# Kernel tuning notes

Hardware: AMD Instinct MI355X
Metric: run time of the kernel (lower is better)

The kernel has to match this reference:

```python
import jax, jax.numpy as jnp
import numpy as np

N = 20000      # nodes
E = 640000     # edges (before self-loops)
F = 64         # base node feature len
H = 2          # heads per layer
EPS = 1e-5
NEG_SLOPE = 0.2  # PyG GATConv leaky_relu slope


def setup_inputs():
    key = jax.random.key(0)
    ks = jax.random.split(key, 16)
    s = 0.1
    x = jax.random.normal(ks[0], (N, F), jnp.float32)
    edge_index = jax.random.randint(ks[1], (2, E), 0, N, dtype=jnp.int64)
    # layer 1: in=F, heads=H, out-per-head C1=F -> out dim H*F=128
    C1 = F
    W1 = jax.random.normal(ks[2], (F, H * C1), jnp.float32) * s
    att_src1 = jax.random.normal(ks[3], (H, C1), jnp.float32) * s
    att_dst1 = jax.random.normal(ks[4], (H, C1), jnp.float32) * s
    bias1 = jnp.zeros((H * C1,), jnp.float32)
    gamma1 = jnp.ones((H * C1,), jnp.float32)
    beta1 = jnp.zeros((H * C1,), jnp.float32)
    # layer 2: in=H*F=128, heads=H, out-per-head C2=H*F -> out dim H*H*F=256
    C2 = H * F
    W2 = jax.random.normal(ks[5], (H * C1, H * C2), jnp.float32) * s
    att_src2 = jax.random.normal(ks[6], (H, C2), jnp.float32) * s
    att_dst2 = jax.random.normal(ks[7], (H, C2), jnp.float32) * s
    bias2 = jnp.zeros((H * C2,), jnp.float32)
    gamma2 = jnp.ones((H * C2,), jnp.float32)
    beta2 = jnp.zeros((H * C2,), jnp.float32)
    return {"x": x, "edge_index": edge_index,
            "W1": W1, "att_src1": att_src1, "att_dst1": att_dst1, "bias1": bias1,
            "gamma1": gamma1, "beta1": beta1,
            "W2": W2, "att_src2": att_src2, "att_dst2": att_dst2, "bias2": bias2,
            "gamma2": gamma2, "beta2": beta2}


def _gat_conv(x, src, dst, W, att_src, att_dst, bias):
    # PyG GATConv (concat=True, add_self_loops already applied to src/dst)
    n = x.shape[0]
    h, c = att_src.shape
    hx = (x @ W).reshape(n, h, c)                       # [N,H,C]
    a_s = jnp.einsum('nhc,hc->nh', hx, att_src)         # [N,H]
    a_d = jnp.einsum('nhc,hc->nh', hx, att_dst)
    e = a_s[src] + a_d[dst]                             # [E',H]
    e = jnp.where(e > 0, e, NEG_SLOPE * e)              # leaky relu
    # segment softmax over incoming edges of each target node
    m = jax.ops.segment_max(e, dst, num_segments=n)     # [N,H]
    p = jnp.exp(e - m[dst])
    z = jax.ops.segment_sum(p, dst, num_segments=n)     # [N,H]
    alpha = p / z[dst]                                  # [E',H]
    msg = hx[src] * alpha[:, :, None]                   # [E',H,C]
    out = jax.ops.segment_sum(msg, dst, num_segments=n) # [N,H,C]
    return out.reshape(n, h * c) + bias


def _batch_norm(x, gamma, beta):
    mu = x.mean(axis=0)
    var = x.var(axis=0)  # biased, matches torch BN normalization
    return (x - mu) * jax.lax.rsqrt(var + EPS) * gamma + beta


def reference(x, edge_index, W1, att_src1, att_dst1, bias1, gamma1, beta1,
              W2, att_src2, att_dst2, bias2, gamma2, beta2):
    loops = jnp.arange(N, dtype=edge_index.dtype)
    src = jnp.concatenate([edge_index[0], loops])
    dst = jnp.concatenate([edge_index[1], loops])
    h = _gat_conv(x, src, dst, W1, att_src1, att_dst1, bias1)
    h = jax.nn.relu(_batch_norm(h, gamma1, beta1))
    h = _gat_conv(h, src, dst, W2, att_src2, att_dst2, bias2)
    h = jax.nn.relu(_batch_norm(h, gamma2, beta2))
    return h
```

## Files before the change

kernel.cpp:

```cpp
#include <hip/hip_runtime.h>
#include <hip/hip_bf16.h>
#include <math.h>

#define NN 20000
#define ER 640000
#define ET 660000
#define HH 2
#define D1 128
#define D2 256
#define EPSV 1e-5f
#define SLOPE 0.2f

typedef __attribute__((ext_vector_type(8))) short bf16x8;
typedef __attribute__((ext_vector_type(4))) float f32x4;


__device__ __forceinline__ int detect64(const void* ei) {
  const int* p = (const int*)ei;
  return (p[1] | p[3] | p[5] | p[7]) == 0;
}
__device__ __forceinline__ int clampn(int v) { return v < 0 ? 0 : (v >= NN ? NN-1 : v); }
__device__ __forceinline__ float bf16_lo(unsigned int u){ return __uint_as_float(u<<16); }
__device__ __forceinline__ float bf16_hi(unsigned int u){ return __uint_as_float(u & 0xffff0000u); }

__global__ void k_front(const void* ei, const float* W1, const float* W2,
                        __hip_bfloat16* W1t, __hip_bfloat16* W2c, int* dpart, int* gcount) {
  extern __shared__ int hist[];
  int b = blockIdx.x, t = threadIdx.x;
  if (b == 0 && t == 0) *gcount = 0;
  if (b < 160) {
    int i = b*256 + t;
    if (i < 8192) {
      int n = i >> 6, k = i & 63;
      W1t[i] = __float2bfloat16(W1[k*128 + n]);
    } else {
      int i2 = i - 8192;
      int kc = i2 >> 13, n = (i2 >> 5) & 255, kk = i2 & 31;
      W2c[i2] = __float2bfloat16(W2[(kc*32 + kk)*256 + n]);
    }
    return;
  }
  int db = b - 160;
  for (int i = t; i < NN; i += 256) hist[i] = 0;
  __syncthreads();
  int is64 = detect64(ei);
  int base = db * 80000;
  if (is64) {
    const long long* p64 = (const long long*)ei;
    for (int i = base + t*4; i < base + 80000; i += 1024) {
      uint4 qa = *(const uint4*)(p64 + ER + i);
      uint4 qb = *(const uint4*)(p64 + ER + i + 2);
      atomicAdd(&hist[clampn((int)qa.x)], 1);
      atomicAdd(&hist[clampn((int)qa.z)], 1);
      atomicAdd(&hist[clampn((int)qb.x)], 1);
      atomicAdd(&hist[clampn((int)qb.z)], 1);
    }
  } else {
    const int* p32 = (const int*)ei;
    for (int i = base + t*4; i < base + 80000; i += 1024) {
      uint4 q = *(const uint4*)(p32 + ER + i);
      atomicAdd(&hist[clampn((int)q.x)], 1);
      atomicAdd(&hist[clampn((int)q.y)], 1);
      atomicAdd(&hist[clampn((int)q.z)], 1);
      atomicAdd(&hist[clampn((int)q.w)], 1);
    }
  }
  __syncthreads();
  for (int i = t; i < NN; i += 256) dpart[db*NN + i] = hist[i];
}

__global__ __launch_bounds__(256) void k_alloc(const int* dpart, int* begv, int* endv,
                                               int* cursor, int* gcount, float* bnz) {
  __shared__ int wsum[4], wbase[4];
  int gid = blockIdx.x*256 + threadIdx.x;
  if (gid < 768) bnz[gid] = 0.f;
  int d = 0;
  if (gid < NN) {
    d = 1;
    #pragma unroll
    for (int bb = 0; bb < 8; bb++) d += dpart[bb*NN + gid];
  }
  int lane = threadIdx.x & 63, w = threadIdx.x >> 6;
  int v = d;
  #pragma unroll
  for (int o = 1; o < 64; o <<= 1) {
    int u = __shfl_up(v, o);
    if (lane >= o) v += u;
  }
  if (lane == 63) wsum[w] = v;
  __syncthreads();
  if (threadIdx.x == 0) {
    int s0 = wsum[0], s1 = wsum[1], s2 = wsum[2], s3 = wsum[3];
    int b = atomicAdd(gcount, s0 + s1 + s2 + s3);
    wbase[0] = b; wbase[1] = b + s0; wbase[2] = b + s0 + s1; wbase[3] = b + s0 + s1 + s2;
  }
  __syncthreads();
  if (gid < NN) {
    int beg = wbase[w] + v - d;
    begv[gid] = beg; cursor[gid] = beg; endv[gid] = beg + d;
  }
}

__global__ void k_scatter(const void* ei, int* cursor, int* srcs) {
  int i0 = (blockIdx.x*256 + threadIdx.x)*4;
  if (i0 >= ET) return;
  int s[4], d[4];
  if (i0 >= ER) {
    #pragma unroll
    for (int k = 0; k < 4; k++) { s[k] = i0 + k - ER; d[k] = s[k]; }
  } else if (detect64(ei)) {
    const long long* p64 = (const long long*)ei;
    uint4 qa = *(const uint4*)(p64 + i0);
    uint4 qb = *(const uint4*)(p64 + i0 + 2);
    uint4 ra = *(const uint4*)(p64 + ER + i0);
    uint4 rb = *(const uint4*)(p64 + ER + i0 + 2);
    s[0]=clampn((int)qa.x); s[1]=clampn((int)qa.z); s[2]=clampn((int)qb.x); s[3]=clampn((int)qb.z);
    d[0]=clampn((int)ra.x); d[1]=clampn((int)ra.z); d[2]=clampn((int)rb.x); d[3]=clampn((int)rb.z);
  } else {
    const int* p32 = (const int*)ei;
    uint4 qs = *(const uint4*)(p32 + i0);
    uint4 qd = *(const uint4*)(p32 + ER + i0);
    s[0]=clampn((int)qs.x); s[1]=clampn((int)qs.y); s[2]=clampn((int)qs.z); s[3]=clampn((int)qs.w);
    d[0]=clampn((int)qd.x); d[1]=clampn((int)qd.y); d[2]=clampn((int)qd.z); d[3]=clampn((int)qd.w);
  }
  #pragma unroll
  for (int k = 0; k < 4; k++) {
    int pos = atomicAdd(&cursor[d[k]], 1);
    srcs[pos] = s[k];
  }
}

__global__ __launch_bounds__(256) void k_gemm1f(const float* x, const __hip_bfloat16* W1t,
                                                const float* att_s1, const float* att_d1,
                                                __hip_bfloat16* hxb, float2* as1, float2* ad1) {
  __shared__ __hip_bfloat16 As[64][72];
  __shared__ __hip_bfloat16 Bs[128][72];
  __shared__ float asred[4][64], adred[4][64];
  int t = threadIdx.x;
  int m0 = blockIdx.x * 64;
  for (int i = t; i < 512; i += 256) {
    int r = i >> 3, s = i & 7;
    int gr = m0 + r; if (gr >= NN) gr = NN - 1;
    float4 f0 = ((const float4*)(x + (size_t)gr*64))[s*2];
    float4 f1 = ((const float4*)(x + (size_t)gr*64))[s*2+1];
    __hip_bfloat16 hb[8] = {
      __float2bfloat16(f0.x), __float2bfloat16(f0.y), __float2bfloat16(f0.z), __float2bfloat16(f0.w),
      __float2bfloat16(f1.x), __float2bfloat16(f1.y), __float2bfloat16(f1.z), __float2bfloat16(f1.w)};
    *(uint4*)&As[r][s*8] = *(uint4*)hb;
  }
  for (int i = t; i < 1024; i += 256) {
    int r = i >> 3, s = i & 7;
    *(uint4*)&Bs[r][s*8] = ((const uint4*)(W1t + (size_t)r*64))[s];
  }
  __syncthreads();
  int w = t >> 6, lane = t & 63;
  int lm = lane & 15, q = lane >> 4;
  f32x4 acc[4][2];
  #pragma unroll
  for (int rt = 0; rt < 4; rt++)
    #pragma unroll
    for (int ct = 0; ct < 2; ct++) acc[rt][ct] = (f32x4){0.f,0.f,0.f,0.f};
  #pragma unroll
  for (int kc = 0; kc < 2; kc++) {
    bf16x8 bfr[2];
    #pragma unroll
    for (int ct = 0; ct < 2; ct++)
      bfr[ct] = *(const bf16x8*)&Bs[w*32 + ct*16 + lm][kc*32 + q*8];
    #pragma unroll
    for (int rt = 0; rt < 4; rt++) {
      bf16x8 a = *(const bf16x8*)&As[rt*16 + lm][kc*32 + q*8];
      acc[rt][0] = __builtin_amdgcn_mfma_f32_16x16x32_bf16(a, bfr[0], acc[rt][0], 0, 0, 0);
      acc[rt][1] = __builtin_amdgcn_mfma_f32_16x16x32_bf16(a, bfr[1], acc[rt][1], 0, 0, 0);
    }
  }
  #pragma unroll
  for (int rt = 0; rt < 4; rt++)
    #pragma unroll
    for (int ct = 0; ct < 2; ct++)
      #pragma unroll
      for (int rg = 0; rg < 4; rg++) {
        int row = m0 + rt*16 + q*4 + rg;
        int col = w*32 + ct*16 + lm;
        if (row < NN) hxb[(size_t)row*128 + col] = __float2bfloat16(acc[rt][ct][rg]);
      }
  float asc[2], adc[2];
  #pragma unroll
  for (int ct = 0; ct < 2; ct++) {
    int col = w*32 + ct*16 + lm;
    asc[ct] = att_s1[col]; adc[ct] = att_d1[col];
  }
  #pragma unroll
  for (int rt = 0; rt < 4; rt++)
    #pragma unroll
    for (int rg = 0; rg < 4; rg++) {
      float ps = acc[rt][0][rg]*asc[0] + acc[rt][1][rg]*asc[1];
      float pd = acc[rt][0][rg]*adc[0] + acc[rt][1][rg]*adc[1];
      #pragma unroll
      for (int o = 1; o < 16; o <<= 1) { ps += __shfl_xor(ps, o); pd += __shfl_xor(pd, o); }
      if (lm == 0) { int row = rt*16 + q*4 + rg; asred[w][row] = ps; adred[w][row] = pd; }
    }
  __syncthreads();
  if (t < 64) {
    int row = m0 + t;
    if (row < NN) {
      as1[row] = make_float2(asred[0][t] + asred[1][t], asred[2][t] + asred[3][t]);
      ad1[row] = make_float2(adred[0][t] + adred[1][t], adred[2][t] + adred[3][t]);
    }
  }
}

__global__ __launch_bounds__(256) void k_gemm2f(const float* out1, const __hip_bfloat16* W2c,
                                                const float* bns1, const float* bnq1,
                                                const float* gamma1, const float* beta1,
                                                const float* att_s2, const float* att_d2,
                                                __hip_bfloat16* hxb, float2* as2, float2* ad2) {
  __shared__ __hip_bfloat16 As[64][136];
  __shared__ __hip_bfloat16 Bs[256][40];
  __shared__ float AB[2][128];
  __shared__ float asred[4][64], adred[4][64];
  int t = threadIdx.x;
  int m0 = blockIdx.x * 64;
  if (t < 128) {
    float mean = bns1[t]*(1.f/NN);
    float var  = bnq1[t]*(1.f/NN) - mean*mean;
    float A = rsqrtf(var + EPSV)*gamma1[t];
    AB[0][t] = A; AB[1][t] = beta1[t] - mean*A;
  }
  __syncthreads();
  for (int i = t; i < 1024; i += 256) {
    int r = i >> 4, s = i & 15;
    int gr = m0 + r; if (gr >= NN) gr = NN - 1;
    float4 f0 = ((const float4*)(out1 + (size_t)gr*128))[s*2];
    float4 f1 = ((const float4*)(out1 + (size_t)gr*128))[s*2+1];
    int c = s*8;
    float v[8] = {f0.x,f0.y,f0.z,f0.w,f1.x,f1.y,f1.z,f1.w};
    __hip_bfloat16 hb[8];
    #pragma unroll
    for (int k = 0; k < 8; k++)
      hb[k] = __float2bfloat16(fmaxf(v[k]*AB[0][c+k] + AB[1][c+k], 0.f));
    *(uint4*)&As[r][s*8] = *(uint4*)hb;
  }
  int w = t >> 6, lane = t & 63;
  int lm = lane & 15, q = lane >> 4;
  f32x4 acc[4][4];
  #pragma unroll
  for (int rt = 0; rt < 4; rt++)
    #pragma unroll
    for (int ct = 0; ct < 4; ct++) acc[rt][ct] = (f32x4){0.f,0.f,0.f,0.f};
  for (int kc = 0; kc < 4; kc++) {
    __syncthreads();
    for (int i = t; i < 1024; i += 256) {
      int r = i >> 2, s = i & 3;
      *(uint4*)&Bs[r][s*8] = ((const uint4*)(W2c + ((size_t)kc*256 + r)*32))[s];
    }
    __syncthreads();
    bf16x8 bfr[4];
    #pragma unroll
    for (int ct = 0; ct < 4; ct++)
      bfr[ct] = *(const bf16x8*)&Bs[w*64 + ct*16 + lm][q*8];
    #pragma unroll
    for (int rt = 0; rt < 4; rt++) {
      bf16x8 a = *(const bf16x8*)&As[rt*16 + lm][kc*32 + q*8];
      #pragma unroll
      for (int ct = 0; ct < 4; ct++)
        acc[rt][ct] = __builtin_amdgcn_mfma_f32_16x16x32_bf16(a, bfr[ct], acc[rt][ct], 0, 0, 0);
    }
  }
  #pragma unroll
  for (int rt = 0; rt < 4; rt++)
    #pragma unroll
    for (int ct = 0; ct < 4; ct++)
      #pragma unroll
      for (int rg = 0; rg < 4; rg++) {
        int row = m0 + rt*16 + q*4 + rg;
        int col = w*64 + ct*16 + lm;
        if (row < NN) hxb[(size_t)row*256 + col] = __float2bfloat16(acc[rt][ct][rg]);
      }
  float asc[4], adc[4];
  #pragma unroll
  for (int ct = 0; ct < 4; ct++) {
    int col = w*64 + ct*16 + lm;
    asc[ct] = att_s2[col]; adc[ct] = att_d2[col];
  }
  #pragma unroll
  for (int rt = 0; rt < 4; rt++)
    #pragma unroll
    for (int rg = 0; rg < 4; rg++) {
      float ps = acc[rt][0][rg]*asc[0] + acc[rt][1][rg]*asc[1]
               + acc[rt][2][rg]*asc[2] + acc[rt][3][rg]*asc[3];
      float pd = acc[rt][0][rg]*adc[0] + acc[rt][1][rg]*adc[1]
               + acc[rt][2][rg]*adc[2] + acc[rt][3][rg]*adc[3];
      #pragma unroll
      for (int o = 1; o < 16; o <<= 1) { ps += __shfl_xor(ps, o); pd += __shfl_xor(pd, o); }
      if (lm == 0) { int row = rt*16 + q*4 + rg; asred[w][row] = ps; adred[w][row] = pd; }
    }
  __syncthreads();
  if (t < 64) {
    int row = m0 + t;
    if (row < NN) {
      as2[row] = make_float2(asred[0][t] + asred[1][t], asred[2][t] + asred[3][t]);
      ad2[row] = make_float2(adred[0][t] + adred[1][t], adred[2][t] + adred[3][t]);
    }
  }
}

__global__ __launch_bounds__(64) void k_agg1(const int* begv, const int* endv, const int* srcs,
                                             const float2* asv, const float2* adv,
                                             const uint2* hx, const float* bias, float* out) {
  __shared__ float2 sp[2][64];
  int n = blockIdx.x, t = threadIdx.x;
  int l = t & 31, eo = t >> 5;
  int h = l >> 4;
  float2 ad = adv[n];
  int beg = begv[n], end = endv[n];
  float a0=0.f,a1=0.f,a2=0.f,a3=0.f,z0=0.f,z1=0.f;
  for (int cb = beg; cb < end; cb += 64) {
    int len = end - cb; if (len > 64) len = 64;
    if (t < len) {
      int s = srcs[cb + t];
      float2 as = asv[s];
      float e0 = as.x + ad.x, e1 = as.y + ad.y;
      e0 = e0 > 0.f ? e0 : SLOPE*e0;
      e1 = e1 > 0.f ? e1 : SLOPE*e1;
      float p0 = __expf(e0), p1 = __expf(e1);
      sp[0][t] = make_float2(__int_as_float(s), p0);
      sp[1][t] = make_float2(__int_as_float(s), p1);
      z0 += p0; z1 += p1;
    }
    __syncthreads();
    for (int j = eo; j < len; j += 2) {
      float2 v = sp[h][j];
      uint2 u = hx[(size_t)__float_as_int(v.x)*32 + l];
      a0 += v.y*bf16_lo(u.x); a1 += v.y*bf16_hi(u.x);
      a2 += v.y*bf16_lo(u.y); a3 += v.y*bf16_hi(u.y);
    }
    __syncthreads();
  }
  a0 += __shfl_down(a0, 32); a1 += __shfl_down(a1, 32);
  a2 += __shfl_down(a2, 32); a3 += __shfl_down(a3, 32);
  #pragma unroll
  for (int o = 1; o < 64; o <<= 1) { z0 += __shfl_xor(z0, o); z1 += __shfl_xor(z1, o); }
  if (t < 32) {
    float inv = 1.f / (h ? z1 : z0);
    float4 b4 = ((const float4*)bias)[t];
    float4 o4 = { a0*inv + b4.x, a1*inv + b4.y, a2*inv + b4.z, a3*inv + b4.w };
    ((float4*)(out + (size_t)n*D1))[t] = o4;
  }
}

__global__ __launch_bounds__(64) void k_agg2(const int* begv, const int* endv, const int* srcs,
                                             const float2* asv, const float2* adv,
                                             const uint2* hx, const float* bias, float* out) {
  __shared__ float2 sp[2][64];
  int n = blockIdx.x, t = threadIdx.x;
  int h = t >> 5;
  float2 ad = adv[n];
  int beg = begv[n], end = endv[n];
  float a0=0.f,a1=0.f,a2=0.f,a3=0.f,z0=0.f,z1=0.f;
  for (int cb = beg; cb < end; cb += 64) {
    int len = end - cb; if (len > 64) len = 64;
    if (t < len) {
      int s = srcs[cb + t];
      float2 as = asv[s];
      float e0 = as.x + ad.x, e1 = as.y + ad.y;
      e0 = e0 > 0.f ? e0 : SLOPE*e0;
      e1 = e1 > 0.f ? e1 : SLOPE*e1;
      float p0 = __expf(e0), p1 = __expf(e1);
      sp[0][t] = make_float2(__int_as_float(s), p0);
      sp[1][t] = make_float2(__int_as_float(s), p1);
      z0 += p0; z1 += p1;
    }
    __syncthreads();
    int j = 0;
    for (; j + 1 < len; j += 2) {
      float2 v0 = sp[h][j], v1 = sp[h][j+1];
      uint2 u0 = hx[(size_t)__float_as_int(v0.x)*64 + t];
      uint2 u1 = hx[(size_t)__float_as_int(v1.x)*64 + t];
      a0 += v0.y*bf16_lo(u0.x) + v1.y*bf16_lo(u1.x);
      a1 += v0.y*bf16_hi(u0.x) + v1.y*bf16_hi(u1.x);
      a2 += v0.y*bf16_lo(u0.y) + v1.y*bf16_lo(u1.y);
      a3 += v0.y*bf16_hi(u0.y) + v1.y*bf16_hi(u1.y);
    }
    for (; j < len; j++) {
      float2 v = sp[h][j];
      uint2 u = hx[(size_t)__float_as_int(v.x)*64 + t];
      a0 += v.y*bf16_lo(u.x); a1 += v.y*bf16_hi(u.x);
      a2 += v.y*bf16_lo(u.y); a3 += v.y*bf16_hi(u.y);
    }
    __syncthreads();
  }
  #pragma unroll
  for (int o = 1; o < 64; o <<= 1) { z0 += __shfl_xor(z0, o); z1 += __shfl_xor(z1, o); }
  float inv = 1.f / (h ? z1 : z0);
  float4 b4 = ((const float4*)bias)[t];
  float4 o4 = { a0*inv + b4.x, a1*inv + b4.y, a2*inv + b4.z, a3*inv + b4.w };
  ((float4*)(out + (size_t)n*D2))[t] = o4;
}

template<int D>
__global__ void k_bnstats(const float* x, float* bnsum, float* bnsq) {
  const int ROWS = 100;
  int c = threadIdx.x;
  int r0 = blockIdx.x * ROWS;
  float s = 0.f, s2 = 0.f;
  for (int r = 0; r < ROWS; r++) {
    float v = x[(size_t)(r0 + r)*D + c];
    s += v; s2 += v*v;
  }
  atomicAdd(&bnsum[c], s);
  atomicAdd(&bnsq[c], s2);
}

__global__ void k_bnapply2(const float* x, const float* bnsum, const float* bnsq,
                           const float* gamma, const float* beta, float* out) {
  int i = blockIdx.x*blockDim.x + threadIdx.x;
  if (i >= NN*D2/4) return;
  int c = (i & 63) * 4;
  float4 v = ((const float4*)x)[i];
  float r[4] = {v.x, v.y, v.z, v.w};
  #pragma unroll
  for (int k = 0; k < 4; k++) {
    float mean = bnsum[c+k] * (1.f/NN);
    float var  = bnsq[c+k] * (1.f/NN) - mean*mean;
    float o = (r[k] - mean) * rsqrtf(var + EPSV) * gamma[c+k] + beta[c+k];
    r[k] = o > 0.f ? o : 0.f;
  }
  float4 o4 = {r[0], r[1], r[2], r[3]};
  ((float4*)out)[i] = o4;
}

extern "C" void kernel_launch(void* const* d_in, const int* in_sizes, int n_in,
                              void* d_out, int out_size, void* d_ws, size_t ws_size,
                              hipStream_t stream) {
  const float* x      = (const float*)d_in[0];
  const void*  ei     = d_in[1];
  const float* W1     = (const float*)d_in[2];
  const float* att_s1 = (const float*)d_in[3];
  const float* att_d1 = (const float*)d_in[4];
  const float* bias1  = (const float*)d_in[5];
  const float* gamma1 = (const float*)d_in[6];
  const float* beta1  = (const float*)d_in[7];
  const float* W2     = (const float*)d_in[8];
  const float* att_s2 = (const float*)d_in[9];
  const float* att_d2 = (const float*)d_in[10];
  const float* bias2  = (const float*)d_in[11];
  const float* gamma2 = (const float*)d_in[12];
  const float* beta2  = (const float*)d_in[13];

  char* p = (char*)d_ws;
  __hip_bfloat16* hx1b = (__hip_bfloat16*)p; p += (size_t)NN*D1*2;
  __hip_bfloat16* hx2b = (__hip_bfloat16*)p; p += (size_t)NN*D2*2;
  __hip_bfloat16* W1t  = (__hip_bfloat16*)p; p += 8192*2;
  __hip_bfloat16* W2c  = (__hip_bfloat16*)p; p += 32768*2;
  float* out1 = (float*)p; p += (size_t)NN*D1*4;
  float* out2 = (float*)p; p += (size_t)NN*D2*4;
  float2* as1 = (float2*)p; p += (size_t)NN*8;
  float2* ad1 = (float2*)p; p += (size_t)NN*8;
  float2* as2 = (float2*)p; p += (size_t)NN*8;
  float2* ad2 = (float2*)p; p += (size_t)NN*8;
  float* bns1 = (float*)p; p += D1*4;
  float* bnq1 = (float*)p; p += D1*4;
  float* bns2 = (float*)p; p += D2*4;
  float* bnq2 = (float*)p; p += D2*4;
  int* dpart  = (int*)p; p += (size_t)8*NN*4;
  int* begv   = (int*)p; p += NN*4;
  int* endv   = (int*)p; p += NN*4;
  int* cursor = (int*)p; p += NN*4;
  int* gcount = (int*)p; p += 16*4;
  int* srcs   = (int*)p; p += (size_t)ET*4;

  k_front<<<168, 256, NN*sizeof(int), stream>>>(ei, W1, W2, W1t, W2c, dpart, gcount);
  k_alloc<<<(NN+255)/256, 256, 0, stream>>>(dpart, begv, endv, cursor, gcount, bns1);
  k_scatter<<<(ET/4 + 255)/256, 256, 0, stream>>>(ei, cursor, srcs);

  k_gemm1f<<<(NN+63)/64, 256, 0, stream>>>(x, W1t, att_s1, att_d1, hx1b, as1, ad1);
  k_agg1<<<NN, 64, 0, stream>>>(begv, endv, srcs, as1, ad1, (const uint2*)hx1b, bias1, out1);
  k_bnstats<D1><<<200, D1, 0, stream>>>(out1, bns1, bnq1);

  k_gemm2f<<<(NN+63)/64, 256, 0, stream>>>(out1, W2c, bns1, bnq1, gamma1, beta1,
                                           att_s2, att_d2, hx2b, as2, ad2);
  k_agg2<<<NN, 64, 0, stream>>>(begv, endv, srcs, as2, ad2, (const uint2*)hx2b, bias2, out2);
  k_bnstats<D2><<<200, D2, 0, stream>>>(out2, bns2, bnq2);
  k_bnapply2<<<(NN*D2/4 + 255)/256, 256, 0, stream>>>(out2, bns2, bnq2, gamma2, beta2,
                                                      (float*)d_out);
}
```

Before: 274.6 us.

## Merge edge scatter into layer-1 GEMM launch and widen aggregation gathers to 16B

Folds the CSR scatter kernel into the layer-1 GEMM kernel as extra blocks, so one launch is saved and the two independent workloads can overlap. Both aggregation kernels now load 8 bf16 per lane with uint4 and process several edges per wavefront in parallel. The partial sums are then combined with shuffles. The aim is fewer, wider gather requests and more memory-level parallelism per node. The cost is more registers and some idle lanes on low-degree nodes.

```diff
diff --git a/kernel.cpp b/kernel.cpp
--- a/kernel.cpp
+++ b/kernel.cpp
@@ -5,15 +5,14 @@
 #define NN 20000
 #define ER 640000
 #define ET 660000
-#define HH 2
 #define D1 128
 #define D2 256
 #define EPSV 1e-5f
 #define SLOPE 0.2f
+#define NT1 313
 
 typedef __attribute__((ext_vector_type(8))) short bf16x8;
 typedef __attribute__((ext_vector_type(4))) float f32x4;
-
 
 __device__ __forceinline__ int detect64(const void* ei) {
   const int* p = (const int*)ei;
@@ -101,43 +100,44 @@
   }
 }
 
-__global__ void k_scatter(const void* ei, int* cursor, int* srcs) {
-  int i0 = (blockIdx.x*256 + threadIdx.x)*4;
-  if (i0 >= ET) return;
-  int s[4], d[4];
-  if (i0 >= ER) {
-    #pragma unroll
-    for (int k = 0; k < 4; k++) { s[k] = i0 + k - ER; d[k] = s[k]; }
-  } else if (detect64(ei)) {
-    const long long* p64 = (const long long*)ei;
-    uint4 qa = *(const uint4*)(p64 + i0);
-    uint4 qb = *(const uint4*)(p64 + i0 + 2);
-    uint4 ra = *(const uint4*)(p64 + ER + i0);
-    uint4 rb = *(const uint4*)(p64 + ER + i0 + 2);
-    s[0]=clampn((int)qa.x); s[1]=clampn((int)qa.z); s[2]=clampn((int)qb.x); s[3]=clampn((int)qb.z);
-    d[0]=clampn((int)ra.x); d[1]=clampn((int)ra.z); d[2]=clampn((int)rb.x); d[3]=clampn((int)rb.z);
-  } else {
-    const int* p32 = (const int*)ei;
-    uint4 qs = *(const uint4*)(p32 + i0);
-    uint4 qd = *(const uint4*)(p32 + ER + i0);
-    s[0]=clampn((int)qs.x); s[1]=clampn((int)qs.y); s[2]=clampn((int)qs.z); s[3]=clampn((int)qs.w);
-    d[0]=clampn((int)qd.x); d[1]=clampn((int)qd.y); d[2]=clampn((int)qd.z); d[3]=clampn((int)qd.w);
-  }
-  #pragma unroll
-  for (int k = 0; k < 4; k++) {
-    int pos = atomicAdd(&cursor[d[k]], 1);
-    srcs[pos] = s[k];
-  }
-}
-
-__global__ __launch_bounds__(256) void k_gemm1f(const float* x, const __hip_bfloat16* W1t,
-                                                const float* att_s1, const float* att_d1,
-                                                __hip_bfloat16* hxb, float2* as1, float2* ad1) {
+__global__ __launch_bounds__(256) void k_gs(const float* x, const __hip_bfloat16* W1t,
+                                            const float* att_s1, const float* att_d1,
+                                            __hip_bfloat16* hxb, float2* as1, float2* ad1,
+                                            const void* ei, int* cursor, int* srcs) {
   __shared__ __hip_bfloat16 As[64][72];
   __shared__ __hip_bfloat16 Bs[128][72];
   __shared__ float asred[4][64], adred[4][64];
-  int t = threadIdx.x;
-  int m0 = blockIdx.x * 64;
+  int b = blockIdx.x, t = threadIdx.x;
+  if (b >= NT1) {
+    int i0 = ((b - NT1)*256 + t)*4;
+    if (i0 >= ET) return;
+    int s[4], d[4];
+    if (i0 >= ER) {
+      #pragma unroll
+      for (int k = 0; k < 4; k++) { s[k] = i0 + k - ER; d[k] = s[k]; }
+    } else if (detect64(ei)) {
+      const long long* p64 = (const long long*)ei;
+      uint4 qa = *(const uint4*)(p64 + i0);
+      uint4 qb = *(const uint4*)(p64 + i0 + 2);
+      uint4 ra = *(const uint4*)(p64 + ER + i0);
+      uint4 rb = *(const uint4*)(p64 + ER + i0 + 2);
+      s[0]=clampn((int)qa.x); s[1]=clampn((int)qa.z); s[2]=clampn((int)qb.x); s[3]=clampn((int)qb.z);
+      d[0]=clampn((int)ra.x); d[1]=clampn((int)ra.z); d[2]=clampn((int)rb.x); d[3]=clampn((int)rb.z);
+    } else {
+      const int* p32 = (const int*)ei;
+      uint4 qs = *(const uint4*)(p32 + i0);
+      uint4 qd = *(const uint4*)(p32 + ER + i0);
+      s[0]=clampn((int)qs.x); s[1]=clampn((int)qs.y); s[2]=clampn((int)qs.z); s[3]=clampn((int)qs.w);
+      d[0]=clampn((int)qd.x); d[1]=clampn((int)qd.y); d[2]=clampn((int)qd.z); d[3]=clampn((int)qd.w);
+    }
+    #pragma unroll
+    for (int k = 0; k < 4; k++) {
+      int pos = atomicAdd(&cursor[d[k]], 1);
+      srcs[pos] = s[k];
+    }
+    return;
+  }
+  int m0 = b * 64;
   for (int i = t; i < 512; i += 256) {
     int r = i >> 3, s = i & 7;
     int gr = m0 + r; if (gr >= NN) gr = NN - 1;
@@ -153,8 +153,7 @@
     *(uint4*)&Bs[r][s*8] = ((const uint4*)(W1t + (size_t)r*64))[s];
   }
   __syncthreads();
-  int w = t >> 6, lane = t & 63;
-  int lm = lane & 15, q = lane >> 4;
+  int w = t >> 6, lane = t & 63, lm = lane & 15, q = lane >> 4;
   f32x4 acc[4][2];
   #pragma unroll
   for (int rt = 0; rt < 4; rt++)
@@ -240,8 +239,7 @@
       hb[k] = __float2bfloat16(fmaxf(v[k]*AB[0][c+k] + AB[1][c+k], 0.f));
     *(uint4*)&As[r][s*8] = *(uint4*)hb;
   }
-  int w = t >> 6, lane = t & 63;
-  int lm = lane & 15, q = lane >> 4;
+  int w = t >> 6, lane = t & 63, lm = lane & 15, q = lane >> 4;
   f32x4 acc[4][4];
   #pragma unroll
   for (int rt = 0; rt < 4; rt++)
@@ -306,14 +304,15 @@
 
 __global__ __launch_bounds__(64) void k_agg1(const int* begv, const int* endv, const int* srcs,
                                              const float2* asv, const float2* adv,
-                                             const uint2* hx, const float* bias, float* out) {
+                                             const uint4* hx, const float* bias, float* out) {
   __shared__ float2 sp[2][64];
   int n = blockIdx.x, t = threadIdx.x;
-  int l = t & 31, eo = t >> 5;
-  int h = l >> 4;
+  int el = t >> 4, c = t & 15;
+  int h = c >> 3;
   float2 ad = adv[n];
   int beg = begv[n], end = endv[n];
-  float a0=0.f,a1=0.f,a2=0.f,a3=0.f,z0=0.f,z1=0.f;
+  float a[8] = {0.f,0.f,0.f,0.f,0.f,0.f,0.f,0.f};
+  float z0 = 0.f, z1 = 0.f;
   for (int cb = beg; cb < end; cb += 64) {
     int len = end - cb; if (len > 64) len = 64;
     if (t < len) {
@@ -328,35 +327,49 @@
       z0 += p0; z1 += p1;
     }
     __syncthreads();
-    for (int j = eo; j < len; j += 2) {
-      float2 v = sp[h][j];
-      uint2 u = hx[(size_t)__float_as_int(v.x)*32 + l];
-      a0 += v.y*bf16_lo(u.x); a1 += v.y*bf16_hi(u.x);
-      a2 += v.y*bf16_lo(u.y); a3 += v.y*bf16_hi(u.y);
+    for (int j = 0; j < len; j += 4) {
+      int e = j + el;
+      if (e < len) {
+        float2 v = sp[h][e];
+        uint4 u = hx[(size_t)__float_as_int(v.x)*16 + c];
+        float pj = v.y;
+        a[0] += pj*bf16_lo(u.x); a[1] += pj*bf16_hi(u.x);
+        a[2] += pj*bf16_lo(u.y); a[3] += pj*bf16_hi(u.y);
+        a[4] += pj*bf16_lo(u.z); a[5] += pj*bf16_hi(u.z);
+        a[6] += pj*bf16_lo(u.w); a[7] += pj*bf16_hi(u.w);
+      }
     }
     __syncthreads();
   }
-  a0 += __shfl_down(a0, 32); a1 += __shfl_down(a1, 32);
-  a2 += __shfl_down(a2, 32); a3 += __shfl_down(a3, 32);
+  #pragma unroll
+  for (int k = 0; k < 8; k++) {
+    a[k] += __shfl_down(a[k], 32);
+    a[k] += __shfl_down(a[k], 16);
+  }
   #pragma unroll
   for (int o = 1; o < 64; o <<= 1) { z0 += __shfl_xor(z0, o); z1 += __shfl_xor(z1, o); }
-  if (t < 32) {
+  if (t < 16) {
     float inv = 1.f / (h ? z1 : z0);
-    float4 b4 = ((const float4*)bias)[t];
-    float4 o4 = { a0*inv + b4.x, a1*inv + b4.y, a2*inv + b4.z, a3*inv + b4.w };
-    ((float4*)(out + (size_t)n*D1))[t] = o4;
+    float4 b0 = ((const float4*)bias)[2*c];
+    float4 b1 = ((const float4*)bias)[2*c+1];
+    float4 o0 = { a[0]*inv + b0.x, a[1]*inv + b0.y, a[2]*inv + b0.z, a[3]*inv + b0.w };
+    float4 o1 = { a[4]*inv + b1.x, a[5]*inv + b1.y, a[6]*inv + b1.z, a[7]*inv + b1.w };
+    ((float4*)(out + (size_t)n*D1))[2*c]   = o0;
+    ((float4*)(out + (size_t)n*D1))[2*c+1] = o1;
   }
 }
 
 __global__ __launch_bounds__(64) void k_agg2(const int* begv, const int* endv, const int* srcs,
                                              const float2* asv, const float2* adv,
-                                             const uint2* hx, const float* bias, float* out) {
+                                             const uint4* hx, const float* bias, float* out) {
   __shared__ float2 sp[2][64];
   int n = blockIdx.x, t = threadIdx.x;
-  int h = t >> 5;
+  int el = t >> 5, c = t & 31;
+  int h = c >> 4;
   float2 ad = adv[n];
   int beg = begv[n], end = endv[n];
-  float a0=0.f,a1=0.f,a2=0.f,a3=0.f,z0=0.f,z1=0.f;
+  float a[8] = {0.f,0.f,0.f,0.f,0.f,0.f,0.f,0.f};
+  float z0 = 0.f, z1 = 0.f;
   for (int cb = beg; cb < end; cb += 64) {
     int len = end - cb; if (len > 64) len = 64;
     if (t < len) {
@@ -371,30 +384,33 @@
       z0 += p0; z1 += p1;
     }
     __syncthreads();
-    int j = 0;
-    for (; j + 1 < len; j += 2) {
-      float2 v0 = sp[h][j], v1 = sp[h][j+1];
-      uint2 u0 = hx[(size_t)__float_as_int(v0.x)*64 + t];
-      uint2 u1 = hx[(size_t)__float_as_int(v1.x)*64 + t];
-      a0 += v0.y*bf16_lo(u0.x) + v1.y*bf16_lo(u1.x);
-      a1 += v0.y*bf16_hi(u0.x) + v1.y*bf16_hi(u1.x);
-      a2 += v0.y*bf16_lo(u0.y) + v1.y*bf16_lo(u1.y);
-      a3 += v0.y*bf16_hi(u0.y) + v1.y*bf16_hi(u1.y);
-    }
-    for (; j < len; j++) {
-      float2 v = sp[h][j];
-      uint2 u = hx[(size_t)__float_as_int(v.x)*64 + t];
-      a0 += v.y*bf16_lo(u.x); a1 += v.y*bf16_hi(u.x);
-      a2 += v.y*bf16_lo(u.y); a3 += v.y*bf16_hi(u.y);
+    for (int j = 0; j < len; j += 2) {
+      int e = j + el;
+      if (e < len) {
+        float2 v = sp[h][e];
+        uint4 u = hx[(size_t)__float_as_int(v.x)*32 + c];
+        float pj = v.y;
+        a[0] += pj*bf16_lo(u.x); a[1] += pj*bf16_hi(u.x);
+        a[2] += pj*bf16_lo(u.y); a[3] += pj*bf16_hi(u.y);
+        a[4] += pj*bf16_lo(u.z); a[5] += pj*bf16_hi(u.z);
+        a[6] += pj*bf16_lo(u.w); a[7] += pj*bf16_hi(u.w);
+      }
     }
     __syncthreads();
   }
   #pragma unroll
+  for (int k = 0; k < 8; k++) a[k] += __shfl_down(a[k], 32);
+  #pragma unroll
   for (int o = 1; o < 64; o <<= 1) { z0 += __shfl_xor(z0, o); z1 += __shfl_xor(z1, o); }
-  float inv = 1.f / (h ? z1 : z0);
-  float4 b4 = ((const float4*)bias)[t];
-  float4 o4 = { a0*inv + b4.x, a1*inv + b4.y, a2*inv + b4.z, a3*inv + b4.w };
-  ((float4*)(out + (size_t)n*D2))[t] = o4;
+  if (t < 32) {
+    float inv = 1.f / (h ? z1 : z0);
+    float4 b0 = ((const float4*)bias)[2*c];
+    float4 b1 = ((const float4*)bias)[2*c+1];
+    float4 o0 = { a[0]*inv + b0.x, a[1]*inv + b0.y, a[2]*inv + b0.z, a[3]*inv + b0.w };
+    float4 o1 = { a[4]*inv + b1.x, a[5]*inv + b1.y, a[6]*inv + b1.z, a[7]*inv + b1.w };
+    ((float4*)(out + (size_t)n*D2))[2*c]   = o0;
+    ((float4*)(out + (size_t)n*D2))[2*c+1] = o1;
+  }
 }
 
 template<int D>
@@ -469,17 +485,18 @@
   int* gcount = (int*)p; p += 16*4;
   int* srcs   = (int*)p; p += (size_t)ET*4;
 
+  const int SCB = (ET/4 + 255)/256;
   k_front<<<168, 256, NN*sizeof(int), stream>>>(ei, W1, W2, W1t, W2c, dpart, gcount);
   k_alloc<<<(NN+255)/256, 256, 0, stream>>>(dpart, begv, endv, cursor, gcount, bns1);
-  k_scatter<<<(ET/4 + 255)/256, 256, 0, stream>>>(ei, cursor, srcs);
-
-  k_gemm1f<<<(NN+63)/64, 256, 0, stream>>>(x, W1t, att_s1, att_d1, hx1b, as1, ad1);
-  k_agg1<<<NN, 64, 0, stream>>>(begv, endv, srcs, as1, ad1, (const uint2*)hx1b, bias1, out1);
+  k_gs<<<NT1 + SCB, 256, 0, stream>>>(x, W1t, att_s1, att_d1, hx1b, as1, ad1,
+                                      ei, cursor, srcs);
+
+  k_agg1<<<NN, 64, 0, stream>>>(begv, endv, srcs, as1, ad1, (const uint4*)hx1b, bias1, out1);
   k_bnstats<D1><<<200, D1, 0, stream>>>(out1, bns1, bnq1);
 
   k_gemm2f<<<(NN+63)/64, 256, 0, stream>>>(out1, W2c, bns1, bnq1, gamma1, beta1,
                                            att_s2, att_d2, hx2b, as2, ad2);
-  k_agg2<<<NN, 64, 0, stream>>>(begv, endv, srcs, as2, ad2, (const uint2*)hx2b, bias2, out2);
+  k_agg2<<<NN, 64, 0, stream>>>(begv, endv, srcs, as2, ad2, (const uint4*)hx2b, bias2, out2);
   k_bnstats<D2><<<200, D2, 0, stream>>>(out2, bns2, bnq2);
   k_bnapply2<<<(NN*D2/4 + 255)/256, 256, 0, stream>>>(out2, bns2, bnq2, gamma2, beta2,
                                                       (float*)d_out);
```

After: 260.4 us. 1.05x faster.
